# Performance work log

Hardware: AMD Instinct MI355X
Metric: run time of the kernel (lower is better)

## Reference

```python
import jax, jax.numpy as jnp
import numpy as np

H = 1024       # hidden_size
VOCAB = 32000  # output_size
L = 128        # max_length
B = 64         # batch


def setup_inputs() -> dict:
    key = jax.random.key(0)
    ks = jax.random.split(key, 16)
    inp = {
        "input_ids": jax.random.randint(ks[0], (1, B), 0, VOCAB),
        "hidden": jax.random.normal(ks[1], (1, B, H), jnp.float32),
        "encoder_outputs": jax.random.normal(ks[2], (L, B, H), jnp.float32),
        # parameters
        "emb": jax.random.normal(ks[3], (VOCAB, H), jnp.float32) * 0.02,
        "attn_W": jax.random.normal(ks[4], (H, 2 * H), jnp.float32) * 0.02,
        "attn_b": jnp.zeros((H,), jnp.float32),
        "v": jax.random.uniform(ks[5], (H,), jnp.float32),
        "w_ih": jax.random.normal(ks[6], (3 * H, 2 * H), jnp.float32) * 0.02,
        "w_hh": jax.random.normal(ks[7], (3 * H, H), jnp.float32) * 0.02,
        "b_ih": jnp.zeros((3 * H,), jnp.float32),
        "b_hh": jnp.zeros((3 * H,), jnp.float32),
        "out_W": jax.random.normal(ks[8], (VOCAB, 3 * H), jnp.float32) * 0.02,
        "out_b": jnp.zeros((VOCAB,), jnp.float32),
    }
    return inp


def reference(input_ids, hidden, encoder_outputs, emb, attn_W, attn_b, v,
              w_ih, w_hh, b_ih, b_hh, out_W, out_b):
    # Dropout in eval mode (identity).
    embedded = emb[input_ids]                      # [1, B, H]
    eo = jnp.transpose(encoder_outputs, (1, 0, 2))  # [B, L, H]
    h0 = hidden[0]                                  # [B, H]

    # Additive (Bahdanau) attention score
    h_rep = jnp.broadcast_to(h0[:, None, :], (eo.shape[0], eo.shape[1], h0.shape[-1]))
    cat = jnp.concatenate([eo, h_rep], axis=-1)     # [B, L, 2H]
    energy = jnp.tanh(jnp.einsum('blk,hk->blh', cat, attn_W) + attn_b)  # [B, L, H]
    scores = jnp.einsum('blh,h->bl', energy, v)     # [B, L]
    attention = jax.nn.softmax(scores, axis=-1)     # [B, L]
    weighted = jnp.einsum('bl,blh->bh', attention, eo)  # [B, H]

    # GRU cell (single layer, single timestep), PyTorch gate order r,z,n
    x = jnp.concatenate([embedded[0], weighted], axis=-1)  # [B, 2H]
    gx = x @ w_ih.T + b_ih                                  # [B, 3H]
    gh = h0 @ w_hh.T + b_hh                                 # [B, 3H]
    xr, xz, xn = jnp.split(gx, 3, axis=-1)
    hr, hz, hn = jnp.split(gh, 3, axis=-1)
    r = jax.nn.sigmoid(xr + hr)
    z = jax.nn.sigmoid(xz + hz)
    n = jnp.tanh(xn + r * hn)
    h_new = (1.0 - z) * n + z * h0                          # [B, H]

    out_cat = jnp.concatenate([h_new, weighted, embedded[0]], axis=-1)  # [B, 3H]
    output = out_cat @ out_W.T + out_b                      # [B, VOCAB]
    return output, h_new[None], attention[:, None, :]
```

## Files before the change

### kernel.cpp

```cpp
#include <hip/hip_runtime.h>
#include <math.h>

#define Hdim 1024
#define VOC 32000
#define LSEQ 128
#define BSZ 64

typedef __attribute__((ext_vector_type(8))) short bf16x8;
typedef __attribute__((ext_vector_type(4))) float f32x4;

__device__ __forceinline__ float fast_tanhf(float x) {
    return 1.0f - 2.0f / (__expf(2.0f * x) + 1.0f);
}
__device__ __forceinline__ float sigmoidf(float x) {
    return 1.0f / (1.0f + __expf(-x));
}
__device__ __forceinline__ short f2bf(float f) {
    unsigned u = __float_as_uint(f);
    unsigned r = (u + 0x7fffu + ((u >> 16) & 1u)) >> 16;
    return (short)r;
}

__device__ __forceinline__ void stage16(const float* __restrict__ src, short* dst) {
    f32x4 v0 = *(const f32x4*)(src);
    f32x4 v1 = *(const f32x4*)(src + 4);
    f32x4 v2 = *(const f32x4*)(src + 8);
    f32x4 v3 = *(const f32x4*)(src + 12);
    bf16x8 p0, p1;
    p0[0] = f2bf(v0[0]); p0[1] = f2bf(v0[1]); p0[2] = f2bf(v0[2]); p0[3] = f2bf(v0[3]);
    p0[4] = f2bf(v1[0]); p0[5] = f2bf(v1[1]); p0[6] = f2bf(v1[2]); p0[7] = f2bf(v1[3]);
    p1[0] = f2bf(v2[0]); p1[1] = f2bf(v2[1]); p1[2] = f2bf(v2[2]); p1[3] = f2bf(v2[3]);
    p1[4] = f2bf(v3[0]); p1[5] = f2bf(v3[1]); p1[6] = f2bf(v3[2]); p1[7] = f2bf(v3[3]);
    *(bf16x8*)(dst) = p0;
    *(bf16x8*)(dst + 8) = p1;
}

__global__ __launch_bounds__(256) void convert_bf16(
    const float* __restrict__ enc, const float* __restrict__ attnW,
    const float* __restrict__ hidden,
    short* __restrict__ enc_bf, short* __restrict__ attnW_bf,
    short* __restrict__ hidden_bf)
{
    const int NG_ENC = (LSEQ * BSZ * Hdim) / 8;
    const int NG_AW  = (Hdim * 2 * Hdim) / 8;
    const int NG_H   = (BSZ * Hdim) / 8;
    const int total = NG_ENC + NG_AW + NG_H;
    for (int g = blockIdx.x * 256 + threadIdx.x; g < total; g += gridDim.x * 256) {
        const float* src; short* dst; int idx;
        if (g < NG_ENC)              { src = enc;    dst = enc_bf;    idx = g; }
        else if (g < NG_ENC + NG_AW) { src = attnW;  dst = attnW_bf;  idx = g - NG_ENC; }
        else                         { src = hidden; dst = hidden_bf; idx = g - NG_ENC - NG_AW; }
        f32x4 a = *(const f32x4*)(src + (size_t)idx * 8);
        f32x4 b = *(const f32x4*)(src + (size_t)idx * 8 + 4);
        bf16x8 p;
        p[0] = f2bf(a[0]); p[1] = f2bf(a[1]); p[2] = f2bf(a[2]); p[3] = f2bf(a[3]);
        p[4] = f2bf(b[0]); p[5] = f2bf(b[1]); p[6] = f2bf(b[2]); p[7] = f2bf(b[3]);
        *(bf16x8*)(dst + (size_t)idx * 8) = p;
    }
}

__global__ __launch_bounds__(256) void ugemm(
    const short* __restrict__ A,
    const short* __restrict__ B,
    float* __restrict__ C)
{
    __shared__ short As[64 * 72];
    __shared__ short Bs[128 * 72];

    const int t = threadIdx.x;
    const int lane = t & 63, wave = t >> 6;
    const int lr = lane & 15, kh = lane >> 4;
    const int n0 = blockIdx.x * 128;
    const int kstart = blockIdx.y * 256;
    float* Cp = C + (size_t)blockIdx.y * (BSZ * Hdim);

    const int ar = t >> 2, ac = (t & 3) * 16;
    const int br = t >> 1, bc = (t & 1) * 32;

    f32x4 acc[4][2] = {};

    for (int k0 = 0; k0 < 256; k0 += 64) {
        const int kg = kstart + k0;
        {
            const short* s = A + (size_t)ar * Hdim + kg + ac;
            *(bf16x8*)(As + ar * 72 + ac)     = *(const bf16x8*)(s);
            *(bf16x8*)(As + ar * 72 + ac + 8) = *(const bf16x8*)(s + 8);
        }
        {
            const short* s = B + (size_t)(n0 + br) * (2 * Hdim) + kg + bc;
            short* d = Bs + br * 72 + bc;
            *(bf16x8*)(d)      = *(const bf16x8*)(s);
            *(bf16x8*)(d + 8)  = *(const bf16x8*)(s + 8);
            *(bf16x8*)(d + 16) = *(const bf16x8*)(s + 16);
            *(bf16x8*)(d + 24) = *(const bf16x8*)(s + 24);
        }
        __syncthreads();
#pragma unroll
        for (int kk = 0; kk < 64; kk += 32) {
            bf16x8 af[4], bfr[2];
#pragma unroll
            for (int mi = 0; mi < 4; ++mi)
                af[mi] = *(const bf16x8*)(As + (mi * 16 + lr) * 72 + kk + kh * 8);
#pragma unroll
            for (int ni = 0; ni < 2; ++ni)
                bfr[ni] = *(const bf16x8*)(Bs + (wave * 32 + ni * 16 + lr) * 72 + kk + kh * 8);
#pragma unroll
            for (int mi = 0; mi < 4; ++mi)
#pragma unroll
                for (int ni = 0; ni < 2; ++ni)
                    acc[mi][ni] = __builtin_amdgcn_mfma_f32_16x16x32_bf16(
                        af[mi], bfr[ni], acc[mi][ni], 0, 0, 0);
        }
        __syncthreads();
    }

#pragma unroll
    for (int mi = 0; mi < 4; ++mi)
#pragma unroll
        for (int ni = 0; ni < 2; ++ni) {
            const int col = n0 + wave * 32 + ni * 16 + lr;
#pragma unroll
            for (int r = 0; r < 4; ++r) {
                const int row = mi * 16 + kh * 4 + r;
                Cp[(size_t)row * Hdim + col] = acc[mi][ni][r];
            }
        }
}

__global__ __launch_bounds__(512) void attn_scores_mfma(
    const short* __restrict__ enc_bf,
    const short* __restrict__ W1_bf,
    const float* __restrict__ u4,
    const float* __restrict__ attnb,
    const float* __restrict__ vvec,
    float* __restrict__ scores_part)
{
    __shared__ short As[128 * 72];
    __shared__ short Bs[128 * 72];
    __shared__ float red[8][64];
    __shared__ float u_lds[64 * 128];

    const int t = threadIdx.x;
    const int lane = t & 63, wave = t >> 6;
    const int wr = wave >> 2, wc = wave & 3;
    const int lr = lane & 15, kh = lane >> 4;
    const int m0 = blockIdx.x * 128;
    const int n0 = blockIdx.y * 128;

    const int srow = t >> 2, scol = (t & 3) * 16;

    for (int i = t; i < 64 * 128; i += 512) {
        const int b = i >> 7, hl = i & 127;
        const size_t g = (size_t)b * Hdim + n0 + hl;
        u_lds[i] = u4[g] + u4[65536 + g] + u4[2 * 65536 + g] + u4[3 * 65536 + g]
                 + attnb[n0 + hl];
    }

    f32x4 acc[4][2] = {};

    for (int kg = 0; kg < Hdim; kg += 64) {
        {
            const short* s = enc_bf + (size_t)(m0 + srow) * Hdim + kg + scol;
            *(bf16x8*)(As + srow * 72 + scol)     = *(const bf16x8*)(s);
            *(bf16x8*)(As + srow * 72 + scol + 8) = *(const bf16x8*)(s + 8);
        }
        {
            const short* s = W1_bf + (size_t)(n0 + srow) * (2 * Hdim) + kg + scol;
            *(bf16x8*)(Bs + srow * 72 + scol)     = *(const bf16x8*)(s);
            *(bf16x8*)(Bs + srow * 72 + scol + 8) = *(const bf16x8*)(s + 8);
        }
        __syncthreads();
#pragma unroll
        for (int kk = 0; kk < 64; kk += 32) {
            bf16x8 af[4], bfr[2];
#pragma unroll
            for (int mi = 0; mi < 4; ++mi)
                af[mi] = *(const bf16x8*)(As + (wr * 64 + mi * 16 + lr) * 72 + kk + kh * 8);
#pragma unroll
            for (int ni = 0; ni < 2; ++ni)
                bfr[ni] = *(const bf16x8*)(Bs + (wc * 32 + ni * 16 + lr) * 72 + kk + kh * 8);
#pragma unroll
            for (int mi = 0; mi < 4; ++mi)
#pragma unroll
                for (int ni = 0; ni < 2; ++ni)
                    acc[mi][ni] = __builtin_amdgcn_mfma_f32_16x16x32_bf16(
                        af[mi], bfr[ni], acc[mi][ni], 0, 0, 0);
        }
        __syncthreads();
    }

    float sv[16];
#pragma unroll
    for (int mi = 0; mi < 4; ++mi)
#pragma unroll
        for (int r = 0; r < 4; ++r) {
            const int lrow = mi * 16 + kh * 4 + r;
            const int b = lrow;
            float s = 0.0f;
#pragma unroll
            for (int ni = 0; ni < 2; ++ni) {
                const int hl = wc * 32 + ni * 16 + lr;
                const float e = fast_tanhf(acc[mi][ni][r] + u_lds[b * 128 + hl]);
                s += e * vvec[n0 + hl];
            }
            sv[mi * 4 + r] = s;
        }
#pragma unroll
    for (int i = 0; i < 16; ++i) {
#pragma unroll
        for (int d = 1; d < 16; d <<= 1)
            sv[i] += __shfl_xor(sv[i], d, 64);
    }
    if (lr == 0) {
#pragma unroll
        for (int mi = 0; mi < 4; ++mi)
#pragma unroll
            for (int r = 0; r < 4; ++r)
                red[wave][mi * 16 + kh * 4 + r] = sv[mi * 4 + r];
    }
    __syncthreads();
    if (t < 128) {
        const int wrr = t >> 6, lrow = t & 63;
        scores_part[(size_t)blockIdx.y * (LSEQ * BSZ) + m0 + t] =
            red[wrr * 4 + 0][lrow] + red[wrr * 4 + 1][lrow] +
            red[wrr * 4 + 2][lrow] + red[wrr * 4 + 3][lrow];
    }
}

__global__ __launch_bounds__(256) void softmax_weighted(
    const float* __restrict__ sp,
    const short* __restrict__ enc_bf,
    const int* __restrict__ ids,
    const float* __restrict__ emb,
    float* __restrict__ attn_out,
    short* __restrict__ x_bf,
    short* __restrict__ oc_bf)
{
    const int b = blockIdx.x, t = threadIdx.x;
    __shared__ float aw[LSEQ];
    __shared__ float red[128];

    {
        const int id = ids[b];
#pragma unroll
        for (int i = 0; i < 4; ++i) {
            const int h = t * 4 + i;
            const short e = f2bf(emb[(size_t)id * Hdim + h]);
            x_bf[(size_t)b * 2048 + h] = e;
            oc_bf[(size_t)b * 3072 + 2048 + h] = e;
        }
    }

    float s = 0.0f;
    if (t < 128) {
#pragma unroll
        for (int g = 0; g < 8; ++g) s += sp[g * (LSEQ * BSZ) + t * 64 + b];
        red[t] = s;
    }
    __syncthreads();
    for (int off = 64; off > 0; off >>= 1) {
        if (t < off) red[t] = fmaxf(red[t], red[t + off]);
        __syncthreads();
    }
    const float mx = red[0];
    __syncthreads();
    float e = 0.0f;
    if (t < 128) { e = __expf(s - mx); red[t] = e; }
    __syncthreads();
    for (int off = 64; off > 0; off >>= 1) {
        if (t < off) red[t] += red[t + off];
        __syncthreads();
    }
    const float inv = 1.0f / red[0];
    if (t < 128) {
        const float p = e * inv;
        aw[t] = p;
        attn_out[(size_t)b * LSEQ + t] = p;
    }
    __syncthreads();

#pragma unroll
    for (int c = 0; c < 2; ++c) {
        const int h = c * 512 + t * 2;
        float a0 = 0.0f, a1 = 0.0f;
        for (int l = 0; l < LSEQ; ++l) {
            const unsigned w = *(const unsigned*)(enc_bf + ((size_t)l * BSZ + b) * Hdim + h);
            const float p = aw[l];
            a0 = fmaf(p, __uint_as_float(w << 16), a0);
            a1 = fmaf(p, __uint_as_float(w & 0xffff0000u), a1);
        }
        const unsigned packed = (unsigned)(unsigned short)f2bf(a0)
                              | ((unsigned)(unsigned short)f2bf(a1) << 16);
        *(unsigned*)(x_bf + (size_t)b * 2048 + 1024 + h) = packed;
        *(unsigned*)(oc_bf + (size_t)b * 3072 + 1024 + h) = packed;
    }
}

__global__ __launch_bounds__(256) void gxgh_gemm(
    const short* __restrict__ x_bf, const float* __restrict__ w_ih,
    const short* __restrict__ hidden_bf, const float* __restrict__ w_hh,
    float* __restrict__ gx4, float* __restrict__ gh4)
{
    __shared__ short As[64 * 72];
    __shared__ short Bs[128 * 72];

    const int t = threadIdx.x;
    const int lane = t & 63, wave = t >> 6;
    const int lr = lane & 15, kh = lane >> 4;

    const short* A; const float* B; float* C; int lda, klen, n0;
    if (blockIdx.x < 24) {
        A = x_bf; B = w_ih; C = gx4; lda = 2048; klen = 512; n0 = blockIdx.x * 128;
    } else {
        A = hidden_bf; B = w_hh; C = gh4; lda = 1024; klen = 256; n0 = (blockIdx.x - 24) * 128;
    }
    const int kstart = blockIdx.y * klen;
    float* Cp = C + (size_t)blockIdx.y * (BSZ * 3 * Hdim);

    const int ar = t >> 2, ac = (t & 3) * 16;
    const int br = t >> 1, bc = (t & 1) * 32;

    f32x4 acc[4][2] = {};

    for (int k0 = 0; k0 < klen; k0 += 64) {
        const int kg = kstart + k0;
        {
            const short* s = A + (size_t)ar * lda + kg + ac;
            *(bf16x8*)(As + ar * 72 + ac)     = *(const bf16x8*)(s);
            *(bf16x8*)(As + ar * 72 + ac + 8) = *(const bf16x8*)(s + 8);
        }
        {
            const float* s = B + (size_t)(n0 + br) * lda + kg + bc;
            stage16(s,      Bs + br * 72 + bc);
            stage16(s + 16, Bs + br * 72 + bc + 16);
        }
        __syncthreads();
#pragma unroll
        for (int kk = 0; kk < 64; kk += 32) {
            bf16x8 af[4], bfr[2];
#pragma unroll
            for (int mi = 0; mi < 4; ++mi)
                af[mi] = *(const bf16x8*)(As + (mi * 16 + lr) * 72 + kk + kh * 8);
#pragma unroll
            for (int ni = 0; ni < 2; ++ni)
                bfr[ni] = *(const bf16x8*)(Bs + (wave * 32 + ni * 16 + lr) * 72 + kk + kh * 8);
#pragma unroll
            for (int mi = 0; mi < 4; ++mi)
#pragma unroll
                for (int ni = 0; ni < 2; ++ni)
                    acc[mi][ni] = __builtin_amdgcn_mfma_f32_16x16x32_bf16(
                        af[mi], bfr[ni], acc[mi][ni], 0, 0, 0);
        }
        __syncthreads();
    }

#pragma unroll
    for (int mi = 0; mi < 4; ++mi)
#pragma unroll
        for (int ni = 0; ni < 2; ++ni) {
            const int col = n0 + wave * 32 + ni * 16 + lr;
#pragma unroll
            for (int r = 0; r < 4; ++r) {
                const int row = mi * 16 + kh * 4 + r;
                Cp[(size_t)row * (3 * Hdim) + col] = acc[mi][ni][r];
            }
        }
}

__global__ __launch_bounds__(256) void gru_kernel(
    const float* __restrict__ gx4, const float* __restrict__ gh4,
    const float* __restrict__ b_ih, const float* __restrict__ b_hh,
    const float* __restrict__ h0,
    float* __restrict__ hnew_out, short* __restrict__ oc_bf)
{
    const int idx = blockIdx.x * 256 + threadIdx.x;
    const int b = idx >> 10, h = idx & 1023;
    const size_t g3 = (size_t)b * (3 * Hdim);
    const size_t P = (size_t)BSZ * 3 * Hdim;
    float xr = b_ih[h], xz = b_ih[Hdim + h], xn = b_ih[2 * Hdim + h];
    float hr = b_hh[h], hz = b_hh[Hdim + h], hn = b_hh[2 * Hdim + h];
#pragma unroll
    for (int s = 0; s < 4; ++s) {
        xr += gx4[s * P + g3 + h];
        xz += gx4[s * P + g3 + Hdim + h];
        xn += gx4[s * P + g3 + 2 * Hdim + h];
        hr += gh4[s * P + g3 + h];
        hz += gh4[s * P + g3 + Hdim + h];
        hn += gh4[s * P + g3 + 2 * Hdim + h];
    }
    const float r = sigmoidf(xr + hr);
    const float z = sigmoidf(xz + hz);
    const float n = fast_tanhf(xn + r * hn);
    const float hv = (1.0f - z) * n + z * h0[(size_t)b * Hdim + h];
    hnew_out[(size_t)b * Hdim + h] = hv;
    oc_bf[g3 + h] = f2bf(hv);
}

__global__ __launch_bounds__(256) void outproj_direct(
    const short* __restrict__ A,
    const float* __restrict__ B,
    const float* __restrict__ bias,
    float* __restrict__ logits)
{
    __shared__ short As[64 * 72];
    __shared__ short Bs[64 * 72];

    const int t = threadIdx.x;
    const int lane = t & 63, wave = t >> 6;
    const int lr = lane & 15, kh = lane >> 4;
    const int n0 = blockIdx.x * 64;
    const int sr = t >> 2, sc = (t & 3) * 16;

    f32x4 acc[4] = {};

    for (int kg = 0; kg < 3072; kg += 64) {
        {
            const short* s = A + (size_t)sr * 3072 + kg + sc;
            *(bf16x8*)(As + sr * 72 + sc)     = *(const bf16x8*)(s);
            *(bf16x8*)(As + sr * 72 + sc + 8) = *(const bf16x8*)(s + 8);
        }
        stage16(B + (size_t)(n0 + sr) * 3072 + kg + sc, Bs + sr * 72 + sc);
        __syncthreads();
#pragma unroll
        for (int kk = 0; kk < 64; kk += 32) {
            bf16x8 af[4], bfr;
#pragma unroll
            for (int mi = 0; mi < 4; ++mi)
                af[mi] = *(const bf16x8*)(As + (mi * 16 + lr) * 72 + kk + kh * 8);
            bfr = *(const bf16x8*)(Bs + (wave * 16 + lr) * 72 + kk + kh * 8);
#pragma unroll
            for (int mi = 0; mi < 4; ++mi)
                acc[mi] = __builtin_amdgcn_mfma_f32_16x16x32_bf16(af[mi], bfr, acc[mi], 0, 0, 0);
        }
        __syncthreads();
    }

    const int col = n0 + wave * 16 + lr;
    const float bb = bias[col];
#pragma unroll
    for (int mi = 0; mi < 4; ++mi)
#pragma unroll
        for (int r = 0; r < 4; ++r) {
            const int row = mi * 16 + kh * 4 + r;
            logits[(size_t)row * VOC + col] = acc[mi][r] + bb;
        }
}

extern "C" void kernel_launch(void* const* d_in, const int* in_sizes, int n_in,
                              void* d_out, int out_size, void* d_ws, size_t ws_size,
                              hipStream_t stream)
{
    const int*   ids    = (const int*)d_in[0];
    const float* hidden = (const float*)d_in[1];
    const float* enc    = (const float*)d_in[2];
    const float* emb    = (const float*)d_in[3];
    const float* attnW  = (const float*)d_in[4];
    const float* attnb  = (const float*)d_in[5];
    const float* vvec   = (const float*)d_in[6];
    const float* w_ih   = (const float*)d_in[7];
    const float* w_hh   = (const float*)d_in[8];
    const float* b_ih   = (const float*)d_in[9];
    const float* b_hh   = (const float*)d_in[10];
    const float* out_W  = (const float*)d_in[11];
    const float* out_b  = (const float*)d_in[12];

    float* out        = (float*)d_out;
    float* out_logits = out;
    float* out_hnew   = out + (size_t)BSZ * VOC;
    float* out_attn   = out_hnew + (size_t)BSZ * Hdim;

    float* ws = (float*)d_ws;
    short* enc_bf    = (short*)ws;
    short* attnW_bf  = (short*)(ws + 4194304);
    short* hidden_bf = (short*)(ws + 5242880);
    float* ws_u4  = ws + 5275648;
    float* ws_sp  = ws_u4 + 262144;
    short* x_bf   = (short*)(ws_sp + 65536);
    short* oc_bf  = (short*)(ws_sp + 131072);
    float* ws_gx4 = ws_sp + 229376;
    float* ws_gh4 = ws_gx4 + 786432;

    convert_bf16<<<dim3(1024), 256, 0, stream>>>(
        enc, attnW, hidden, enc_bf, attnW_bf, hidden_bf);

    ugemm<<<dim3(Hdim / 128, 4), 256, 0, stream>>>(
        hidden_bf, attnW_bf + Hdim, ws_u4);

    attn_scores_mfma<<<dim3(LSEQ / 2, 8), 512, 0, stream>>>(
        enc_bf, attnW_bf, ws_u4, attnb, vvec, ws_sp);

    softmax_weighted<<<dim3(BSZ), 256, 0, stream>>>(
        ws_sp, enc_bf, ids, emb, out_attn, x_bf, oc_bf);

    gxgh_gemm<<<dim3(48, 4), 256, 0, stream>>>(
        x_bf, w_ih, hidden_bf, w_hh, ws_gx4, ws_gh4);

    gru_kernel<<<dim3(BSZ * Hdim / 256), 256, 0, stream>>>(
        ws_gx4, ws_gh4, b_ih, b_hh, hidden, out_hnew, oc_bf);

    outproj_direct<<<dim3(VOC / 64), 256, 0, stream>>>(
        oc_bf, out_W, out_b, out_logits);
}
```

Baseline: 190.0 us.

## Use direct global-to-LDS loads, split softmax across H, prefetch outproj tiles

Three independent changes. The attention-score GEMM now stages tiles with global_load_lds (16-byte direct-to-LDS) into unpadded 64-wide rows, which removes the register round trip but may bring back LDS bank conflicts. The softmax/weighted-sum kernel is split across 4 H-groups with 128 threads each, giving more blocks for the bandwidth-bound reduction at the cost of recomputing the softmax in every group. The output projection prefetches the next K tile into registers before the MFMA loop, so the global loads of out_W overlap with compute.

Result: faster. 185.9 us (-2.2%).

```diff
diff --git a/kernel.cpp b/kernel.cpp
--- a/kernel.cpp
+++ b/kernel.cpp
@@ -19,6 +19,12 @@
     unsigned u = __float_as_uint(f);
     unsigned r = (u + 0x7fffu + ((u >> 16) & 1u)) >> 16;
     return (short)r;
+}
+
+__device__ __forceinline__ void gl_lds16(const short* g, short* l) {
+    __builtin_amdgcn_global_load_lds(
+        (const __attribute__((address_space(1))) unsigned*)g,
+        (__attribute__((address_space(3))) unsigned*)l, 16, 0, 0);
 }
 
 __device__ __forceinline__ void stage16(const float* __restrict__ src, short* dst) {
@@ -135,8 +141,8 @@
     const float* __restrict__ vvec,
     float* __restrict__ scores_part)
 {
-    __shared__ short As[128 * 72];
-    __shared__ short Bs[128 * 72];
+    __shared__ short As[128 * 64];
+    __shared__ short Bs[128 * 64];
     __shared__ float red[8][64];
     __shared__ float u_lds[64 * 128];
 
@@ -147,7 +153,10 @@
     const int m0 = blockIdx.x * 128;
     const int n0 = blockIdx.y * 128;
 
-    const int srow = t >> 2, scol = (t & 3) * 16;
+    const int o1 = t * 16;
+    const int o2 = 8192 + t * 16;
+    const int r1 = o1 >> 7, c1 = (o1 & 127) >> 1;
+    const int r2 = o2 >> 7, c2 = (o2 & 127) >> 1;
 
     for (int i = t; i < 64 * 128; i += 512) {
         const int b = i >> 7, hl = i & 127;
@@ -159,26 +168,20 @@
     f32x4 acc[4][2] = {};
 
     for (int kg = 0; kg < Hdim; kg += 64) {
-        {
-            const short* s = enc_bf + (size_t)(m0 + srow) * Hdim + kg + scol;
-            *(bf16x8*)(As + srow * 72 + scol)     = *(const bf16x8*)(s);
-            *(bf16x8*)(As + srow * 72 + scol + 8) = *(const bf16x8*)(s + 8);
-        }
-        {
-            const short* s = W1_bf + (size_t)(n0 + srow) * (2 * Hdim) + kg + scol;
-            *(bf16x8*)(Bs + srow * 72 + scol)     = *(const bf16x8*)(s);
-            *(bf16x8*)(Bs + srow * 72 + scol + 8) = *(const bf16x8*)(s + 8);
-        }
+        gl_lds16(enc_bf + (size_t)(m0 + r1) * Hdim + kg + c1, As + (o1 >> 1));
+        gl_lds16(enc_bf + (size_t)(m0 + r2) * Hdim + kg + c2, As + (o2 >> 1));
+        gl_lds16(W1_bf + (size_t)(n0 + r1) * (2 * Hdim) + kg + c1, Bs + (o1 >> 1));
+        gl_lds16(W1_bf + (size_t)(n0 + r2) * (2 * Hdim) + kg + c2, Bs + (o2 >> 1));
         __syncthreads();
 #pragma unroll
         for (int kk = 0; kk < 64; kk += 32) {
             bf16x8 af[4], bfr[2];
 #pragma unroll
             for (int mi = 0; mi < 4; ++mi)
-                af[mi] = *(const bf16x8*)(As + (wr * 64 + mi * 16 + lr) * 72 + kk + kh * 8);
+                af[mi] = *(const bf16x8*)(As + (wr * 64 + mi * 16 + lr) * 64 + kk + kh * 8);
 #pragma unroll
             for (int ni = 0; ni < 2; ++ni)
-                bfr[ni] = *(const bf16x8*)(Bs + (wc * 32 + ni * 16 + lr) * 72 + kk + kh * 8);
+                bfr[ni] = *(const bf16x8*)(Bs + (wc * 32 + ni * 16 + lr) * 64 + kk + kh * 8);
 #pragma unroll
             for (int mi = 0; mi < 4; ++mi)
 #pragma unroll
@@ -227,7 +230,7 @@
     }
 }
 
-__global__ __launch_bounds__(256) void softmax_weighted(
+__global__ __launch_bounds__(128) void softmax_weighted(
     const float* __restrict__ sp,
     const short* __restrict__ enc_bf,
     const int* __restrict__ ids,
@@ -236,27 +239,26 @@
     short* __restrict__ x_bf,
     short* __restrict__ oc_bf)
 {
-    const int b = blockIdx.x, t = threadIdx.x;
+    const int b = blockIdx.x, hg = blockIdx.y, t = threadIdx.x;
     __shared__ float aw[LSEQ];
-    __shared__ float red[128];
-
-    {
+    __shared__ float red[LSEQ];
+
+    if (hg == 0) {
         const int id = ids[b];
-#pragma unroll
-        for (int i = 0; i < 4; ++i) {
-            const int h = t * 4 + i;
-            const short e = f2bf(emb[(size_t)id * Hdim + h]);
-            x_bf[(size_t)b * 2048 + h] = e;
-            oc_bf[(size_t)b * 3072 + 2048 + h] = e;
-        }
+        const int h = t * 8;
+        f32x4 e0 = *(const f32x4*)(emb + (size_t)id * Hdim + h);
+        f32x4 e1 = *(const f32x4*)(emb + (size_t)id * Hdim + h + 4);
+        bf16x8 p;
+        p[0] = f2bf(e0[0]); p[1] = f2bf(e0[1]); p[2] = f2bf(e0[2]); p[3] = f2bf(e0[3]);
+        p[4] = f2bf(e1[0]); p[5] = f2bf(e1[1]); p[6] = f2bf(e1[2]); p[7] = f2bf(e1[3]);
+        *(bf16x8*)(x_bf + (size_t)b * 2048 + h) = p;
+        *(bf16x8*)(oc_bf + (size_t)b * 3072 + 2048 + h) = p;
     }
 
     float s = 0.0f;
-    if (t < 128) {
-#pragma unroll
-        for (int g = 0; g < 8; ++g) s += sp[g * (LSEQ * BSZ) + t * 64 + b];
-        red[t] = s;
-    }
+#pragma unroll
+    for (int g = 0; g < 8; ++g) s += sp[g * (LSEQ * BSZ) + t * 64 + b];
+    red[t] = s;
     __syncthreads();
     for (int off = 64; off > 0; off >>= 1) {
         if (t < off) red[t] = fmaxf(red[t], red[t + off]);
@@ -264,36 +266,31 @@
     }
     const float mx = red[0];
     __syncthreads();
-    float e = 0.0f;
-    if (t < 128) { e = __expf(s - mx); red[t] = e; }
+    const float e = __expf(s - mx);
+    red[t] = e;
     __syncthreads();
     for (int off = 64; off > 0; off >>= 1) {
         if (t < off) red[t] += red[t + off];
         __syncthreads();
     }
-    const float inv = 1.0f / red[0];
-    if (t < 128) {
-        const float p = e * inv;
-        aw[t] = p;
-        attn_out[(size_t)b * LSEQ + t] = p;
-    }
+    const float p = e / red[0];
+    aw[t] = p;
+    if (hg == 0) attn_out[(size_t)b * LSEQ + t] = p;
     __syncthreads();
 
-#pragma unroll
-    for (int c = 0; c < 2; ++c) {
-        const int h = c * 512 + t * 2;
-        float a0 = 0.0f, a1 = 0.0f;
-        for (int l = 0; l < LSEQ; ++l) {
-            const unsigned w = *(const unsigned*)(enc_bf + ((size_t)l * BSZ + b) * Hdim + h);
-            const float p = aw[l];
-            a0 = fmaf(p, __uint_as_float(w << 16), a0);
-            a1 = fmaf(p, __uint_as_float(w & 0xffff0000u), a1);
-        }
-        const unsigned packed = (unsigned)(unsigned short)f2bf(a0)
-                              | ((unsigned)(unsigned short)f2bf(a1) << 16);
-        *(unsigned*)(x_bf + (size_t)b * 2048 + 1024 + h) = packed;
-        *(unsigned*)(oc_bf + (size_t)b * 3072 + 1024 + h) = packed;
-    }
+    const int h = hg * 256 + t * 2;
+    float a0 = 0.0f, a1 = 0.0f;
+#pragma unroll 8
+    for (int l = 0; l < LSEQ; ++l) {
+        const unsigned w = *(const unsigned*)(enc_bf + ((size_t)l * BSZ + b) * Hdim + h);
+        const float pw = aw[l];
+        a0 = fmaf(pw, __uint_as_float(w << 16), a0);
+        a1 = fmaf(pw, __uint_as_float(w & 0xffff0000u), a1);
+    }
+    const unsigned packed = (unsigned)(unsigned short)f2bf(a0)
+                          | ((unsigned)(unsigned short)f2bf(a1) << 16);
+    *(unsigned*)(x_bf + (size_t)b * 2048 + 1024 + h) = packed;
+    *(unsigned*)(oc_bf + (size_t)b * 3072 + 1024 + h) = packed;
 }
 
 __global__ __launch_bounds__(256) void gxgh_gemm(
@@ -411,16 +408,42 @@
     const int n0 = blockIdx.x * 64;
     const int sr = t >> 2, sc = (t & 3) * 16;
 
+    const short* Arow = A + (size_t)sr * 3072 + sc;
+    const float* Brow = B + (size_t)(n0 + sr) * 3072 + sc;
+
     f32x4 acc[4] = {};
 
-    for (int kg = 0; kg < 3072; kg += 64) {
+    bf16x8 pa0 = *(const bf16x8*)(Arow);
+    bf16x8 pa1 = *(const bf16x8*)(Arow + 8);
+    f32x4 pb0 = *(const f32x4*)(Brow);
+    f32x4 pb1 = *(const f32x4*)(Brow + 4);
+    f32x4 pb2 = *(const f32x4*)(Brow + 8);
+    f32x4 pb3 = *(const f32x4*)(Brow + 12);
+
+    for (int kt = 0; kt < 48; ++kt) {
+        *(bf16x8*)(As + sr * 72 + sc)     = pa0;
+        *(bf16x8*)(As + sr * 72 + sc + 8) = pa1;
         {
-            const short* s = A + (size_t)sr * 3072 + kg + sc;
-            *(bf16x8*)(As + sr * 72 + sc)     = *(const bf16x8*)(s);
-            *(bf16x8*)(As + sr * 72 + sc + 8) = *(const bf16x8*)(s + 8);
-        }
-        stage16(B + (size_t)(n0 + sr) * 3072 + kg + sc, Bs + sr * 72 + sc);
-        __syncthreads();
+            bf16x8 q0, q1;
+            q0[0] = f2bf(pb0[0]); q0[1] = f2bf(pb0[1]); q0[2] = f2bf(pb0[2]); q0[3] = f2bf(pb0[3]);
+            q0[4] = f2bf(pb1[0]); q0[5] = f2bf(pb1[1]); q0[6] = f2bf(pb1[2]); q0[7] = f2bf(pb1[3]);
+            q1[0] = f2bf(pb2[0]); q1[1] = f2bf(pb2[1]); q1[2] = f2bf(pb2[2]); q1[3] = f2bf(pb2[3]);
+            q1[4] = f2bf(pb3[0]); q1[5] = f2bf(pb3[1]); q1[6] = f2bf(pb3[2]); q1[7] = f2bf(pb3[3]);
+            *(bf16x8*)(Bs + sr * 72 + sc)     = q0;
+            *(bf16x8*)(Bs + sr * 72 + sc + 8) = q1;
+        }
+        __syncthreads();
+
+        if (kt + 1 < 48) {
+            const int kn = (kt + 1) * 64;
+            pa0 = *(const bf16x8*)(Arow + kn);
+            pa1 = *(const bf16x8*)(Arow + kn + 8);
+            pb0 = *(const f32x4*)(Brow + kn);
+            pb1 = *(const f32x4*)(Brow + kn + 4);
+            pb2 = *(const f32x4*)(Brow + kn + 8);
+            pb3 = *(const f32x4*)(Brow + kn + 12);
+        }
+
 #pragma unroll
         for (int kk = 0; kk < 64; kk += 32) {
             bf16x8 af[4], bfr;
@@ -489,7 +512,7 @@
     attn_scores_mfma<<<dim3(LSEQ / 2, 8), 512, 0, stream>>>(
         enc_bf, attnW_bf, ws_u4, attnb, vvec, ws_sp);
 
-    softmax_weighted<<<dim3(BSZ), 256, 0, stream>>>(
+    softmax_weighted<<<dim3(BSZ, 4), 128, 0, stream>>>(
         ws_sp, enc_bf, ids, emb, out_attn, x_bf, oc_bf);
 
     gxgh_gemm<<<dim3(48, 4), 256, 0, stream>>>(
```
